# Optimization experiments

Hardware: AMD Instinct MI355X
Metric: run time of the kernel (lower is better)

The kernel has to match this reference:

```python
import jax, jax.numpy as jnp
import numpy as np

B, A, C, H, W, T = 64, 5, 80, 52, 52, 32
L_COORD, L_OBJ, L_NOOBJ = 5.0, 1.0, 0.5


def setup_inputs():
    key = jax.random.key(0)
    ks = jax.random.split(key, 7)
    pred_cls = jax.random.normal(ks[0], (B, A * C, H, W), jnp.float32)
    pred_response = jax.random.normal(ks[1], (B, A, H, W), jnp.float32)
    pred_bboxes = jax.random.normal(ks[2], (B, A * 4, H, W), jnp.float32)
    # distinct (anchor, y, x) cells per image so scatter writes never collide
    perm = jax.vmap(lambda k: jax.random.permutation(k, A * H * W))(jax.random.split(ks[3], B))[:, :T]
    tgt_idx_box = (perm // (H * W)).astype(jnp.int32)
    tgt_idx_y = ((perm // W) % H).astype(jnp.int32)
    tgt_idx_x = (perm % W).astype(jnp.int32)
    txy = jax.random.uniform(ks[4], (B, T, 2), jnp.float32)  # cell-relative center in (0,1)
    twh = jax.random.uniform(ks[5], (B, T, 2), jnp.float32, minval=0.5, maxval=6.0)  # w,h in cells
    tgt_box = jnp.concatenate([txy, twh], axis=-1)  # [B,T,4] = (tx,ty,tw,th)
    tgt_label = jax.random.randint(ks[6], (B, T), 0, C)
    return {"pred_cls": pred_cls, "pred_response": pred_response, "pred_bboxes": pred_bboxes,
            "tgt_box": tgt_box, "tgt_idx_x": tgt_idx_x, "tgt_idx_y": tgt_idx_y,
            "tgt_idx_box": tgt_idx_box, "tgt_label": tgt_label}


def _bce(x, t):  # binary_cross_entropy_with_logits, elementwise
    return jax.nn.softplus(x) - x * t


def reference(pred_cls, pred_response, pred_bboxes, tgt_box, tgt_idx_x, tgt_idx_y, tgt_idx_box, tgt_label):
    f32 = pred_cls.dtype
    pb = pred_bboxes.reshape(B, A, 4, H, W)  # channel layout a*4+c, matches torch view(-1,4)
    grid_x = jnp.arange(W, dtype=f32)            # broadcasts over last dim
    grid_y = jnp.arange(H, dtype=f32)[:, None]   # broadcasts over H dim
    pw, ph = pb[:, :, 2], pb[:, :, 3]            # raw wh (no exp), as in source
    px1 = jax.nn.sigmoid(pb[:, :, 0]) + grid_x - pw * 0.5  # [B,A,H,W]
    py1 = jax.nn.sigmoid(pb[:, :, 1]) + grid_y - ph * 0.5
    px2, py2 = px1 + pw, py1 + ph
    tx, ty, tw, th = tgt_box[..., 0], tgt_box[..., 1], tgt_box[..., 2], tgt_box[..., 3]  # [B,T]
    cx = tx + tgt_idx_x.astype(f32)
    cy = ty + tgt_idx_y.astype(f32)
    gx1, gy1 = cx - tw * 0.5, cy - th * 0.5
    gx2, gy2 = gx1 + tw, gy1 + th
    e = lambda a: a[:, :, None, None, None]  # [B,T] -> [B,T,1,1,1]
    p = lambda a: a[:, None]                 # [B,A,H,W] -> [B,1,A,H,W]
    dx = jnp.maximum(jnp.minimum(p(px2), e(gx2)) - jnp.maximum(p(px1), e(gx1)), 0.0)
    dy = jnp.maximum(jnp.minimum(p(py2), e(gy2)) - jnp.maximum(p(py1), e(gy1)), 0.0)
    inter = dx * dy
    iou = inter / (p(pw * ph) + e(tw * th) - inter)  # [B,T,A,H,W]
    iou = jax.lax.stop_gradient(iou)  # torch computes IoU under no_grad
    bidx = jnp.arange(B)[:, None]
    tidx = jnp.arange(T)[None, :]
    neg_mask = iou[:, -1] < 0.6  # [B,A,H,W]
    iou_sel = iou[bidx, tidx, tgt_idx_box, tgt_idx_y, tgt_idx_x]  # [B,T]
    gt_response = jnp.zeros((B, A, H, W), f32).at[bidx, tgt_idx_box, tgt_idx_y, tgt_idx_x].set(iou_sel)
    pos_mask = jnp.zeros((B, A, H, W), bool).at[bidx, tgt_idx_box, tgt_idx_y, tgt_idx_x].set(True)
    # per-target coord / class losses
    pbm = pb.transpose(0, 1, 3, 4, 2)  # [B,A,H,W,4]
    pred_off = pbm[bidx, tgt_idx_box, tgt_idx_y, tgt_idx_x]  # [B,T,4]
    loss_xy = _bce(pred_off[..., :2], tgt_box[..., :2]).sum()
    loss_wh = ((pred_off[..., 2:] - tgt_box[..., 2:]) ** 2).sum()
    pcm = pred_cls.reshape(B, A, C, H, W).transpose(0, 1, 3, 4, 2)  # [B,A,H,W,C]
    logits = pcm[bidx, tgt_idx_box, tgt_idx_y, tgt_idx_x]  # [B,T,C]
    logp = jax.nn.log_softmax(logits, axis=-1)
    loss_cls = -jnp.take_along_axis(logp, tgt_label[..., None], axis=-1).sum()
    # objectness losses
    bce_resp = _bce(pred_response, gt_response)
    loss_pos = jnp.where(pos_mask, bce_resp, 0.0).sum() * L_OBJ
    loss_neg = jnp.where(neg_mask & ~pos_mask, bce_resp, 0.0).sum() * L_NOOBJ
    # order: [pObj, nObj, cls, xy, wh]
    return jnp.stack([loss_pos, loss_neg, loss_cls, loss_xy, loss_wh * L_COORD]) / B
```

## Files before the change

### kernel.cpp

```cpp
#include <hip/hip_runtime.h>
#include <math.h>

#define Bn 64
#define An 5
#define Cn 80
#define Hn 52
#define Wn 52
#define Tn 32
#define HWn (Hn * Wn)

#define NB_CELL 1024
#define NB_TGT  512


__device__ __forceinline__ float softplusf_(float x) {
    return fmaxf(x, 0.f) + log1pf(expf(-fabsf(x)));
}

__device__ __forceinline__ float sigmoidf_(float x) {
    return 1.f / (1.f + expf(-x));
}

__device__ __forceinline__ float iou_cell(float pb0, float pb1, float pw, float ph,
                                          int h, int w,
                                          float gx1, float gy1, float gx2, float gy2,
                                          float tarea) {
    float px1 = sigmoidf_(pb0) + (float)w - pw * 0.5f;
    float py1 = sigmoidf_(pb1) + (float)h - ph * 0.5f;
    float px2 = px1 + pw, py2 = py1 + ph;
    float dx = fmaxf(fminf(px2, gx2) - fmaxf(px1, gx1), 0.f);
    float dy = fmaxf(fminf(py2, gy2) - fmaxf(py1, gy1), 0.f);
    float inter = dx * dy;
    return inter / (pw * ph + tarea - inter);
}

__global__ void cell_kernel(const float* __restrict__ pred_resp,
                            const float* __restrict__ pred_bb,
                            const float* __restrict__ tgt_box,
                            const int* __restrict__ tix,
                            const int* __restrict__ tiy,
                            double* __restrict__ cell_part) {
    float acc = 0.f;
    const int total = Bn * An * HWn;
    for (int idx = blockIdx.x * blockDim.x + threadIdx.x; idx < total;
         idx += blockDim.x * NB_CELL) {
        int b = idx / (An * HWn);
        int rem = idx - b * (An * HWn);
        int a = rem / HWn;
        int hw = rem - a * HWn;
        int h = hw / Wn;
        int w = hw - h * Wn;
        int tb = b * Tn + (Tn - 1);
        float tx = tgt_box[tb * 4 + 0], ty = tgt_box[tb * 4 + 1];
        float tw = tgt_box[tb * 4 + 2], th = tgt_box[tb * 4 + 3];
        float cx = tx + (float)tix[tb];
        float cy = ty + (float)tiy[tb];
        float gx1 = cx - tw * 0.5f, gy1 = cy - th * 0.5f;
        float gx2 = gx1 + tw, gy2 = gy1 + th;
        const float* pbb = pred_bb + ((size_t)(b * An + a) * 4) * HWn + hw;
        float pb0 = pbb[0];
        float pb1 = pbb[HWn];
        float pw  = pbb[2 * HWn];
        float ph  = pbb[3 * HWn];
        float iou = iou_cell(pb0, pb1, pw, ph, h, w, gx1, gy1, gx2, gy2, tw * th);
        if (iou < 0.6f) acc += softplusf_(pred_resp[idx]);
    }
    for (int off = 32; off > 0; off >>= 1) acc += __shfl_down(acc, off);
    __shared__ float s[4];
    int lane = threadIdx.x & 63, wid = threadIdx.x >> 6;
    if (lane == 0) s[wid] = acc;
    __syncthreads();
    if (threadIdx.x == 0) {
        cell_part[blockIdx.x] = (double)(s[0] + s[1] + s[2] + s[3]);
    }
}

__global__ void target_kernel(const float* __restrict__ pred_cls,
                              const float* __restrict__ pred_resp,
                              const float* __restrict__ pred_bb,
                              const float* __restrict__ tgt_box,
                              const int* __restrict__ tix,
                              const int* __restrict__ tiy,
                              const int* __restrict__ tib,
                              const int* __restrict__ tlab,
                              double* __restrict__ tgt_part) {
    int wid = threadIdx.x >> 6;
    int lane = threadIdx.x & 63;
    int gwave = blockIdx.x * 4 + wid;
    int b = gwave / Tn;
    int t = gwave - b * Tn;
    int tb = b * Tn + t;
    int abox = tib[tb];
    int y = tiy[tb];
    int x = tix[tb];
    int label = tlab[tb];
    float tx = tgt_box[tb * 4 + 0], ty = tgt_box[tb * 4 + 1];
    float tw = tgt_box[tb * 4 + 2], th = tgt_box[tb * 4 + 3];

    const float* cl = pred_cls + ((size_t)b * (An * Cn) + (size_t)abox * Cn) * HWn + (size_t)y * Wn + x;
    float l0 = cl[(size_t)lane * HWn];
    float l1 = (lane < Cn - 64) ? cl[(size_t)(lane + 64) * HWn] : -INFINITY;
    float m = fmaxf(l0, l1);
    for (int off = 32; off > 0; off >>= 1) m = fmaxf(m, __shfl_xor(m, off));
    float se = expf(l0 - m) + ((lane < Cn - 64) ? expf(l1 - m) : 0.f);
    for (int off = 32; off > 0; off >>= 1) se += __shfl_xor(se, off);
    float lsel = (label < 64) ? __shfl(l0, label) : __shfl(l1, label - 64);
    float loss_cls = m + logf(se) - lsel;

    __shared__ float sm[4][5];
    if (lane == 0) {
        int hw = y * Wn + x;
        const float* pbb = pred_bb + ((size_t)(b * An + abox) * 4) * HWn + hw;
        float pb0 = pbb[0];
        float pb1 = pbb[HWn];
        float pw  = pbb[2 * HWn];
        float ph  = pbb[3 * HWn];
        float r = pred_resp[(size_t)(b * An + abox) * HWn + hw];
        float sp_r = softplusf_(r);

        float cx = tx + (float)x, cy = ty + (float)y;
        float gx1 = cx - tw * 0.5f, gy1 = cy - th * 0.5f;
        float gx2 = gx1 + tw, gy2 = gy1 + th;
        float iou_sel = iou_cell(pb0, pb1, pw, ph, y, x, gx1, gy1, gx2, gy2, tw * th);
        float pos = sp_r - r * iou_sel;

        int tb31 = b * Tn + (Tn - 1);
        float t31x = tgt_box[tb31 * 4 + 0], t31y = tgt_box[tb31 * 4 + 1];
        float t31w = tgt_box[tb31 * 4 + 2], t31h = tgt_box[tb31 * 4 + 3];
        float c31x = t31x + (float)tix[tb31];
        float c31y = t31y + (float)tiy[tb31];
        float g1x = c31x - t31w * 0.5f, g1y = c31y - t31h * 0.5f;
        float g2x = g1x + t31w, g2y = g1y + t31h;
        float iou31 = iou_cell(pb0, pb1, pw, ph, y, x, g1x, g1y, g2x, g2y, t31w * t31h);
        float negcorr = (iou31 < 0.6f) ? sp_r : 0.f;

        float lxy = (softplusf_(pb0) - pb0 * tx) + (softplusf_(pb1) - pb1 * ty);
        float lwh = (pw - tw) * (pw - tw) + (ph - th) * (ph - th);

        sm[wid][0] = pos;
        sm[wid][1] = negcorr;
        sm[wid][2] = loss_cls;
        sm[wid][3] = lxy;
        sm[wid][4] = lwh;
    }
    __syncthreads();
    if (threadIdx.x < 5) {
        int k = threadIdx.x;
        tgt_part[(size_t)k * NB_TGT + blockIdx.x] =
            (double)sm[0][k] + (double)sm[1][k] + (double)sm[2][k] + (double)sm[3][k];
    }
}

__global__ void finalize_kernel(const double* __restrict__ ws, float* __restrict__ out) {
    int lane = threadIdx.x;
    const double* cell_part = ws;
    const double* tgt_part = ws + NB_CELL;

    double c = 0.0;
    for (int i = lane; i < NB_CELL; i += 64) c += cell_part[i];
    double tk[5];
    for (int k = 0; k < 5; ++k) {
        double v = 0.0;
        for (int i = lane; i < NB_TGT; i += 64) v += tgt_part[(size_t)k * NB_TGT + i];
        tk[k] = v;
    }
    for (int off = 32; off > 0; off >>= 1) {
        c += __shfl_down(c, off);
        for (int k = 0; k < 5; ++k) tk[k] += __shfl_down(tk[k], off);
    }
    if (lane == 0) {
        out[0] = (float)(tk[0] / Bn);
        out[1] = (float)(0.5 * (c - tk[1]) / Bn);
        out[2] = (float)(tk[2] / Bn);
        out[3] = (float)(tk[3] / Bn);
        out[4] = (float)(5.0 * tk[4] / Bn);
    }
}

extern "C" void kernel_launch(void* const* d_in, const int* in_sizes, int n_in,
                              void* d_out, int out_size, void* d_ws, size_t ws_size,
                              hipStream_t stream) {
    const float* pred_cls  = (const float*)d_in[0];
    const float* pred_resp = (const float*)d_in[1];
    const float* pred_bb   = (const float*)d_in[2];
    const float* tgt_box   = (const float*)d_in[3];
    const int*   tix       = (const int*)d_in[4];
    const int*   tiy       = (const int*)d_in[5];
    const int*   tib       = (const int*)d_in[6];
    const int*   tlab      = (const int*)d_in[7];
    double* ws = (double*)d_ws;
    float* out = (float*)d_out;

    cell_kernel<<<NB_CELL, 256, 0, stream>>>(pred_resp, pred_bb, tgt_box, tix, tiy, ws);
    target_kernel<<<NB_TGT, 256, 0, stream>>>(pred_cls, pred_resp, pred_bb,
                                              tgt_box, tix, tiy, tib, tlab, ws + NB_CELL);
    finalize_kernel<<<1, 64, 0, stream>>>(ws, out);
}
```

Measured before the change: 353.8 us.

## Fuse cell and target kernels into one launch with float4 cell loads

Merges the per-cell negative-objectness kernel and the per-target kernel into one launch, picking the role by block index. The cell branch now handles four adjacent cells per thread with float4 loads, sized so the grid covers every cell exactly with no grid-stride loop. The finalize kernel uses 256 threads and a shared-memory reduction. This removes a launch and improves load width, but the mixed grid depends on the exact problem shape being divisible by 4.

```diff
diff --git a/kernel.cpp b/kernel.cpp
--- a/kernel.cpp
+++ b/kernel.cpp
@@ -9,8 +9,9 @@
 #define Tn 32
 #define HWn (Hn * Wn)
 
-#define NB_CELL 1024
 #define NB_TGT  512
+#define NB_CELL 845
+#define NB_TOT  (NB_TGT + NB_CELL)
 
 
 __device__ __forceinline__ float softplusf_(float x) {
@@ -34,22 +35,93 @@
     return inter / (pw * ph + tarea - inter);
 }
 
-__global__ void cell_kernel(const float* __restrict__ pred_resp,
-                            const float* __restrict__ pred_bb,
-                            const float* __restrict__ tgt_box,
-                            const int* __restrict__ tix,
-                            const int* __restrict__ tiy,
-                            double* __restrict__ cell_part) {
-    float acc = 0.f;
-    const int total = Bn * An * HWn;
-    for (int idx = blockIdx.x * blockDim.x + threadIdx.x; idx < total;
-         idx += blockDim.x * NB_CELL) {
-        int b = idx / (An * HWn);
-        int rem = idx - b * (An * HWn);
+__global__ void fused_kernel(const float* __restrict__ pred_cls,
+                             const float* __restrict__ pred_resp,
+                             const float* __restrict__ pred_bb,
+                             const float* __restrict__ tgt_box,
+                             const int* __restrict__ tix,
+                             const int* __restrict__ tiy,
+                             const int* __restrict__ tib,
+                             const int* __restrict__ tlab,
+                             double* __restrict__ ws) {
+    int wid = threadIdx.x >> 6;
+    int lane = threadIdx.x & 63;
+
+    if (blockIdx.x < NB_TGT) {
+        int gwave = blockIdx.x * 4 + wid;
+        int b = gwave / Tn;
+        int t = gwave - b * Tn;
+        int tb = b * Tn + t;
+        int abox = tib[tb];
+        int y = tiy[tb];
+        int x = tix[tb];
+        int label = tlab[tb];
+        float tx = tgt_box[tb * 4 + 0], ty = tgt_box[tb * 4 + 1];
+        float tw = tgt_box[tb * 4 + 2], th = tgt_box[tb * 4 + 3];
+
+        const float* cl = pred_cls + ((size_t)b * (An * Cn) + (size_t)abox * Cn) * HWn + (size_t)y * Wn + x;
+        float l0 = cl[(size_t)lane * HWn];
+        float l1 = (lane < Cn - 64) ? cl[(size_t)(lane + 64) * HWn] : -INFINITY;
+        float m = fmaxf(l0, l1);
+        for (int off = 32; off > 0; off >>= 1) m = fmaxf(m, __shfl_xor(m, off));
+        float se = expf(l0 - m) + ((lane < Cn - 64) ? expf(l1 - m) : 0.f);
+        for (int off = 32; off > 0; off >>= 1) se += __shfl_xor(se, off);
+        float lsel = (label < 64) ? __shfl(l0, label) : __shfl(l1, label - 64);
+        float loss_cls = m + logf(se) - lsel;
+
+        __shared__ float sm[4][5];
+        if (lane == 0) {
+            int hw = y * Wn + x;
+            const float* pbb = pred_bb + ((size_t)(b * An + abox) * 4) * HWn + hw;
+            float pb0 = pbb[0];
+            float pb1 = pbb[HWn];
+            float pw  = pbb[2 * HWn];
+            float ph  = pbb[3 * HWn];
+            float r = pred_resp[(size_t)(b * An + abox) * HWn + hw];
+            float sp_r = softplusf_(r);
+
+            float cx = tx + (float)x, cy = ty + (float)y;
+            float gx1 = cx - tw * 0.5f, gy1 = cy - th * 0.5f;
+            float gx2 = gx1 + tw, gy2 = gy1 + th;
+            float iou_sel = iou_cell(pb0, pb1, pw, ph, y, x, gx1, gy1, gx2, gy2, tw * th);
+            float pos = sp_r - r * iou_sel;
+
+            int tb31 = b * Tn + (Tn - 1);
+            float t31x = tgt_box[tb31 * 4 + 0], t31y = tgt_box[tb31 * 4 + 1];
+            float t31w = tgt_box[tb31 * 4 + 2], t31h = tgt_box[tb31 * 4 + 3];
+            float c31x = t31x + (float)tix[tb31];
+            float c31y = t31y + (float)tiy[tb31];
+            float g1x = c31x - t31w * 0.5f, g1y = c31y - t31h * 0.5f;
+            float g2x = g1x + t31w, g2y = g1y + t31h;
+            float iou31 = iou_cell(pb0, pb1, pw, ph, y, x, g1x, g1y, g2x, g2y, t31w * t31h);
+            float negcorr = (iou31 < 0.6f) ? sp_r : 0.f;
+
+            float lxy = (softplusf_(pb0) - pb0 * tx) + (softplusf_(pb1) - pb1 * ty);
+            float lwh = (pw - tw) * (pw - tw) + (ph - th) * (ph - th);
+
+            sm[wid][0] = pos;
+            sm[wid][1] = negcorr;
+            sm[wid][2] = loss_cls;
+            sm[wid][3] = lxy;
+            sm[wid][4] = lwh;
+        }
+        __syncthreads();
+        if (threadIdx.x < 5) {
+            int k = threadIdx.x;
+            ws[NB_CELL + (size_t)k * NB_TGT + blockIdx.x] =
+                (double)sm[0][k] + (double)sm[1][k] + (double)sm[2][k] + (double)sm[3][k];
+        }
+    } else {
+        int cb = blockIdx.x - NB_TGT;
+        int g = cb * 256 + threadIdx.x;
+        int idx0 = g * 4;
+        int b = idx0 / (An * HWn);
+        int rem = idx0 - b * (An * HWn);
         int a = rem / HWn;
         int hw = rem - a * HWn;
         int h = hw / Wn;
-        int w = hw - h * Wn;
+        int w0 = hw - h * Wn;
+
         int tb = b * Tn + (Tn - 1);
         float tx = tgt_box[tb * 4 + 0], ty = tgt_box[tb * 4 + 1];
         float tw = tgt_box[tb * 4 + 2], th = tgt_box[tb * 4 + 3];
@@ -57,123 +129,79 @@
         float cy = ty + (float)tiy[tb];
         float gx1 = cx - tw * 0.5f, gy1 = cy - th * 0.5f;
         float gx2 = gx1 + tw, gy2 = gy1 + th;
-        const float* pbb = pred_bb + ((size_t)(b * An + a) * 4) * HWn + hw;
-        float pb0 = pbb[0];
-        float pb1 = pbb[HWn];
-        float pw  = pbb[2 * HWn];
-        float ph  = pbb[3 * HWn];
-        float iou = iou_cell(pb0, pb1, pw, ph, h, w, gx1, gy1, gx2, gy2, tw * th);
-        if (iou < 0.6f) acc += softplusf_(pred_resp[idx]);
-    }
-    for (int off = 32; off > 0; off >>= 1) acc += __shfl_down(acc, off);
-    __shared__ float s[4];
-    int lane = threadIdx.x & 63, wid = threadIdx.x >> 6;
-    if (lane == 0) s[wid] = acc;
-    __syncthreads();
-    if (threadIdx.x == 0) {
-        cell_part[blockIdx.x] = (double)(s[0] + s[1] + s[2] + s[3]);
-    }
-}
-
-__global__ void target_kernel(const float* __restrict__ pred_cls,
-                              const float* __restrict__ pred_resp,
-                              const float* __restrict__ pred_bb,
-                              const float* __restrict__ tgt_box,
-                              const int* __restrict__ tix,
-                              const int* __restrict__ tiy,
-                              const int* __restrict__ tib,
-                              const int* __restrict__ tlab,
-                              double* __restrict__ tgt_part) {
-    int wid = threadIdx.x >> 6;
-    int lane = threadIdx.x & 63;
-    int gwave = blockIdx.x * 4 + wid;
-    int b = gwave / Tn;
-    int t = gwave - b * Tn;
-    int tb = b * Tn + t;
-    int abox = tib[tb];
-    int y = tiy[tb];
-    int x = tix[tb];
-    int label = tlab[tb];
-    float tx = tgt_box[tb * 4 + 0], ty = tgt_box[tb * 4 + 1];
-    float tw = tgt_box[tb * 4 + 2], th = tgt_box[tb * 4 + 3];
-
-    const float* cl = pred_cls + ((size_t)b * (An * Cn) + (size_t)abox * Cn) * HWn + (size_t)y * Wn + x;
-    float l0 = cl[(size_t)lane * HWn];
-    float l1 = (lane < Cn - 64) ? cl[(size_t)(lane + 64) * HWn] : -INFINITY;
-    float m = fmaxf(l0, l1);
-    for (int off = 32; off > 0; off >>= 1) m = fmaxf(m, __shfl_xor(m, off));
-    float se = expf(l0 - m) + ((lane < Cn - 64) ? expf(l1 - m) : 0.f);
-    for (int off = 32; off > 0; off >>= 1) se += __shfl_xor(se, off);
-    float lsel = (label < 64) ? __shfl(l0, label) : __shfl(l1, label - 64);
-    float loss_cls = m + logf(se) - lsel;
-
-    __shared__ float sm[4][5];
-    if (lane == 0) {
-        int hw = y * Wn + x;
-        const float* pbb = pred_bb + ((size_t)(b * An + abox) * 4) * HWn + hw;
-        float pb0 = pbb[0];
-        float pb1 = pbb[HWn];
-        float pw  = pbb[2 * HWn];
-        float ph  = pbb[3 * HWn];
-        float r = pred_resp[(size_t)(b * An + abox) * HWn + hw];
-        float sp_r = softplusf_(r);
-
-        float cx = tx + (float)x, cy = ty + (float)y;
-        float gx1 = cx - tw * 0.5f, gy1 = cy - th * 0.5f;
-        float gx2 = gx1 + tw, gy2 = gy1 + th;
-        float iou_sel = iou_cell(pb0, pb1, pw, ph, y, x, gx1, gy1, gx2, gy2, tw * th);
-        float pos = sp_r - r * iou_sel;
-
-        int tb31 = b * Tn + (Tn - 1);
-        float t31x = tgt_box[tb31 * 4 + 0], t31y = tgt_box[tb31 * 4 + 1];
-        float t31w = tgt_box[tb31 * 4 + 2], t31h = tgt_box[tb31 * 4 + 3];
-        float c31x = t31x + (float)tix[tb31];
-        float c31y = t31y + (float)tiy[tb31];
-        float g1x = c31x - t31w * 0.5f, g1y = c31y - t31h * 0.5f;
-        float g2x = g1x + t31w, g2y = g1y + t31h;
-        float iou31 = iou_cell(pb0, pb1, pw, ph, y, x, g1x, g1y, g2x, g2y, t31w * t31h);
-        float negcorr = (iou31 < 0.6f) ? sp_r : 0.f;
-
-        float lxy = (softplusf_(pb0) - pb0 * tx) + (softplusf_(pb1) - pb1 * ty);
-        float lwh = (pw - tw) * (pw - tw) + (ph - th) * (ph - th);
-
-        sm[wid][0] = pos;
-        sm[wid][1] = negcorr;
-        sm[wid][2] = loss_cls;
-        sm[wid][3] = lxy;
-        sm[wid][4] = lwh;
-    }
-    __syncthreads();
-    if (threadIdx.x < 5) {
-        int k = threadIdx.x;
-        tgt_part[(size_t)k * NB_TGT + blockIdx.x] =
-            (double)sm[0][k] + (double)sm[1][k] + (double)sm[2][k] + (double)sm[3][k];
+        float tarea = tw * th;
+
+        const float* plane = pred_bb + ((size_t)(b * An + a) * 4) * HWn + hw;
+        float4 v0 = *(const float4*)(plane);
+        float4 v1 = *(const float4*)(plane + HWn);
+        float4 v2 = *(const float4*)(plane + 2 * HWn);
+        float4 v3 = *(const float4*)(plane + 3 * HWn);
+        float4 rr = *(const float4*)(pred_resp + (size_t)(b * An + a) * HWn + hw);
+
+        float acc = 0.f;
+        {
+            float iou = iou_cell(v0.x, v1.x, v2.x, v3.x, h, w0 + 0, gx1, gy1, gx2, gy2, tarea);
+            if (iou < 0.6f) acc += softplusf_(rr.x);
+        }
+        {
+            float iou = iou_cell(v0.y, v1.y, v2.y, v3.y, h, w0 + 1, gx1, gy1, gx2, gy2, tarea);
+            if (iou < 0.6f) acc += softplusf_(rr.y);
+        }
+        {
+            float iou = iou_cell(v0.z, v1.z, v2.z, v3.z, h, w0 + 2, gx1, gy1, gx2, gy2, tarea);
+            if (iou < 0.6f) acc += softplusf_(rr.z);
+        }
+        {
+            float iou = iou_cell(v0.w, v1.w, v2.w, v3.w, h, w0 + 3, gx1, gy1, gx2, gy2, tarea);
+            if (iou < 0.6f) acc += softplusf_(rr.w);
+        }
+
+        for (int off = 32; off > 0; off >>= 1) acc += __shfl_down(acc, off);
+        __shared__ float s[4];
+        if (lane == 0) s[wid] = acc;
+        __syncthreads();
+        if (threadIdx.x == 0) {
+            ws[cb] = (double)(s[0] + s[1] + s[2] + s[3]);
+        }
     }
 }
 
 __global__ void finalize_kernel(const double* __restrict__ ws, float* __restrict__ out) {
-    int lane = threadIdx.x;
+    int tid = threadIdx.x;
+    int lane = tid & 63, wid = tid >> 6;
     const double* cell_part = ws;
     const double* tgt_part = ws + NB_CELL;
 
     double c = 0.0;
-    for (int i = lane; i < NB_CELL; i += 64) c += cell_part[i];
+    for (int i = tid; i < NB_CELL; i += 256) c += cell_part[i];
     double tk[5];
     for (int k = 0; k < 5; ++k) {
         double v = 0.0;
-        for (int i = lane; i < NB_TGT; i += 64) v += tgt_part[(size_t)k * NB_TGT + i];
+        for (int i = tid; i < NB_TGT; i += 256) v += tgt_part[(size_t)k * NB_TGT + i];
         tk[k] = v;
     }
     for (int off = 32; off > 0; off >>= 1) {
         c += __shfl_down(c, off);
         for (int k = 0; k < 5; ++k) tk[k] += __shfl_down(tk[k], off);
     }
+    __shared__ double sd[4][6];
     if (lane == 0) {
-        out[0] = (float)(tk[0] / Bn);
-        out[1] = (float)(0.5 * (c - tk[1]) / Bn);
-        out[2] = (float)(tk[2] / Bn);
-        out[3] = (float)(tk[3] / Bn);
-        out[4] = (float)(5.0 * tk[4] / Bn);
+        sd[wid][0] = c;
+        for (int k = 0; k < 5; ++k) sd[wid][k + 1] = tk[k];
+    }
+    __syncthreads();
+    if (tid == 0) {
+        double cc = sd[0][0] + sd[1][0] + sd[2][0] + sd[3][0];
+        double t0 = sd[0][1] + sd[1][1] + sd[2][1] + sd[3][1];
+        double t1 = sd[0][2] + sd[1][2] + sd[2][2] + sd[3][2];
+        double t2 = sd[0][3] + sd[1][3] + sd[2][3] + sd[3][3];
+        double t3 = sd[0][4] + sd[1][4] + sd[2][4] + sd[3][4];
+        double t4 = sd[0][5] + sd[1][5] + sd[2][5] + sd[3][5];
+        out[0] = (float)(t0 / Bn);
+        out[1] = (float)(0.5 * (cc - t1) / Bn);
+        out[2] = (float)(t2 / Bn);
+        out[3] = (float)(t3 / Bn);
+        out[4] = (float)(5.0 * t4 / Bn);
     }
 }
 
@@ -191,8 +219,7 @@
     double* ws = (double*)d_ws;
     float* out = (float*)d_out;
 
-    cell_kernel<<<NB_CELL, 256, 0, stream>>>(pred_resp, pred_bb, tgt_box, tix, tiy, ws);
-    target_kernel<<<NB_TGT, 256, 0, stream>>>(pred_cls, pred_resp, pred_bb,
-                                              tgt_box, tix, tiy, tib, tlab, ws + NB_CELL);
-    finalize_kernel<<<1, 64, 0, stream>>>(ws, out);
-}
+    fused_kernel<<<NB_TOT, 256, 0, stream>>>(pred_cls, pred_resp, pred_bb,
+                                             tgt_box, tix, tiy, tib, tlab, ws);
+    finalize_kernel<<<1, 256, 0, stream>>>(ws, out);
+}
```

Result: faster. 341.4 us (-3.5%).
